# Kernel tuning notes

Hardware: AMD Instinct MI355X
Metric: run time of the kernel (lower is better)

## Reference

```python
import jax, jax.numpy as jnp
import numpy as np

N_NODES = 50000
N_EDGES = 640000
D = 128      # node feature dim
ED = 128     # edge feature dim
H = 128      # MLP hidden dim


def _glorot(key, shape):
    fan_in = shape[0]
    return jax.random.normal(key, shape, jnp.float32) * (1.0 / np.sqrt(fan_in))


def setup_inputs() -> dict:
    key = jax.random.key(0)
    ks = jax.random.split(key, 12)
    x = jax.random.normal(ks[0], (N_NODES, D), jnp.float32)
    edge_index = jax.random.randint(ks[1], (2, N_EDGES), 0, N_NODES, jnp.int64)
    edge_attr = jax.random.normal(ks[2], (N_EDGES, ED), jnp.float32)
    # edge_model: MLP on concat([src, dest, edge_attr]) -> ED
    We1 = _glorot(ks[3], (2 * D + ED, H)); be1 = jnp.zeros((H,), jnp.float32)
    We2 = _glorot(ks[4], (H, ED));         be2 = jnp.zeros((ED,), jnp.float32)
    # node_model: MLP on concat([x, scatter_mean(edge_attr, row)]) -> D
    Wn1 = _glorot(ks[5], (D + ED, H));     bn1 = jnp.zeros((H,), jnp.float32)
    Wn2 = _glorot(ks[6], (H, D));          bn2 = jnp.zeros((D,), jnp.float32)
    return {"x": x, "edge_index": edge_index, "edge_attr": edge_attr,
            "We1": We1, "be1": be1, "We2": We2, "be2": be2,
            "Wn1": Wn1, "bn1": bn1, "Wn2": Wn2, "bn2": bn2}


def reference(x, edge_index, edge_attr, We1, be1, We2, be2, Wn1, bn1, Wn2, bn2):
    row = edge_index[0]  # source / aggregation target, [E]
    col = edge_index[1]  # destination, [E]
    # edge_model(x[row], x[col], edge_attr): concat -> 2-layer ReLU MLP
    e_in = jnp.concatenate([x[row], x[col], edge_attr], axis=1)  # [E, 2D+ED]
    edge_out = jax.nn.relu(e_in @ We1 + be1) @ We2 + be2          # [E, ED]
    # node_model: scatter-mean of edge messages onto row nodes
    agg = jax.ops.segment_sum(edge_out, row, num_segments=N_NODES)         # [N, ED]
    cnt = jax.ops.segment_sum(jnp.ones((edge_out.shape[0], 1), x.dtype),
                              row, num_segments=N_NODES)                    # [N, 1]
    mean = agg / jnp.maximum(cnt, 1.0)
    n_in = jnp.concatenate([x, mean], axis=1)                     # [N, D+ED]
    x_out = jax.nn.relu(n_in @ Wn1 + bn1) @ Wn2 + bn2             # [N, D]
    return (x_out, edge_out)
```

## Files before the change

### kernel.cpp

```cpp
#include <hip/hip_runtime.h>
#include <stdint.h>


#define E_EDGES 640000
#define N_NODES 50000
#define DIM 128

typedef unsigned short u16;
typedef unsigned int u32x4 __attribute__((ext_vector_type(4)));
typedef float f32x4 __attribute__((ext_vector_type(4)));
typedef short s16x8 __attribute__((ext_vector_type(8)));
union U16 { u32x4 u; s16x8 s; u16 h[8]; };

__device__ __forceinline__ float b2f(u16 u) {
  union { unsigned i; float f; } v; v.i = ((unsigned)u) << 16; return v.f;
}
__device__ __forceinline__ u16 f2b(float f) {
  union { float f; unsigned u; } v; v.f = f;
  unsigned r = v.u + 0x7FFFu + ((v.u >> 16) & 1u);
  return (u16)(r >> 16);
}
__device__ __forceinline__ float ldf(const void* p, long long i, int isF32) {
  return isF32 ? ((const float*)p)[i] : b2f(((const u16*)p)[i]);
}

__global__ void detect_kernel(const void* x, const void* ei, int* flags) {
  __shared__ int sBig, sNz;
  if (threadIdx.x == 0) { sBig = 0; sNz = 0; }
  __syncthreads();
  const u16* xu = (const u16*)x;
  const int* ew = (const int*)ei;
  int big = 0, nz = 0;
  for (int i = threadIdx.x; i < 4096; i += 256) {
    u16 u = xu[2 * i];
    if (((u >> 7) & 0xFF) >= 0x90) big = 1;
    if (ew[2 * i + 1] != 0) nz = 1;
  }
  if (big) atomicOr(&sBig, 1);
  if (nz) atomicOr(&sNz, 1);
  __syncthreads();
  if (threadIdx.x == 0) { flags[0] = sBig; flags[1] = sNz ? 0 : 1; }
}

__global__ void normalize_idx(const void* ei, const int* __restrict__ flags,
                              int* __restrict__ out) {
  int i = blockIdx.x * 256 + threadIdx.x;
  if (flags[1]) out[i] = (int)((const long long*)ei)[i];
  else          out[i] = ((const int*)ei)[i];
}

__global__ void prep_weights(const void* We1, const void* be1, const void* We2,
                             const void* be2, const void* Wn1, const void* bn1,
                             const void* Wn2, const void* bn2,
                             const int* __restrict__ flags,
                             u16* __restrict__ WT1, u16* __restrict__ WT2,
                             u16* __restrict__ WnT1, u16* __restrict__ WnT2,
                             float* __restrict__ biasf) {
  const int isF32 = flags[0];
  int tid = blockIdx.x * 256 + threadIdx.x;
  if (tid < 384 * 128) { int k = tid >> 7, n = tid & 127; WT1 [n * 384 + k] = f2b(ldf(We1, tid, isF32)); }
  if (tid < 128 * 128) { int k = tid >> 7, n = tid & 127; WT2 [n * 128 + k] = f2b(ldf(We2, tid, isF32)); }
  if (tid < 256 * 128) { int k = tid >> 7, n = tid & 127; WnT1[n * 256 + k] = f2b(ldf(Wn1, tid, isF32)); }
  if (tid < 128 * 128) { int k = tid >> 7, n = tid & 127; WnT2[n * 128 + k] = f2b(ldf(Wn2, tid, isF32)); }
  if (tid < 128) {
    biasf[tid]       = ldf(be1, tid, isF32);
    biasf[128 + tid] = ldf(be2, tid, isF32);
    biasf[256 + tid] = ldf(bn1, tid, isF32);
    biasf[384 + tid] = ldf(bn2, tid, isF32);
  }
}

__global__ void convert_x(const void* x, const int* __restrict__ flags,
                          u16* __restrict__ xb) {
  int i = blockIdx.x * 256 + threadIdx.x;
  xb[i] = flags[0] ? f2b(((const float*)x)[i]) : ((const u16*)x)[i];
}

__global__ __launch_bounds__(256) void edge_kernel(
    const u16* __restrict__ xb, const int* __restrict__ ei, const void* ea,
    const u16* __restrict__ WT1, const u16* __restrict__ WT2,
    const float* __restrict__ biasf, const int* __restrict__ flags,
    void* d_out, float* __restrict__ agg, float* __restrict__ cnt) {
  __shared__ u16 h[4][32 * 136];
  const int isF32 = flags[0];
  const int wid = threadIdx.x >> 6, lane = threadIdx.x & 63;
  const int lm = lane & 15, quad = lane >> 4;
  const int ebase = (blockIdx.x * 4 + wid) * 32;

  if (threadIdx.x < 128)
    atomicAdd(&cnt[ei[blockIdx.x * 128 + threadIdx.x]], 1.0f);

  const int e0 = ebase + lm, e1 = ebase + 16 + lm;
  const int row0 = ei[e0], col0 = ei[E_EDGES + e0];
  const int row1 = ei[e1], col1 = ei[E_EDGES + e1];

  const f32x4 fz = {0.f, 0.f, 0.f, 0.f};
  f32x4 acc[2][8];
#pragma unroll
  for (int mt = 0; mt < 2; ++mt)
#pragma unroll
    for (int t = 0; t < 8; ++t) acc[mt][t] = fz;

#pragma unroll
  for (int ks = 0; ks < 12; ++ks) {
    const int k0 = ks * 32 + quad * 8;
    U16 a0, a1;
    if (k0 < 256) {
      const u16 *p0, *p1;
      if (k0 < 128) { p0 = xb + (size_t)row0 * DIM + k0;         p1 = xb + (size_t)row1 * DIM + k0; }
      else          { p0 = xb + (size_t)col0 * DIM + (k0 - 128); p1 = xb + (size_t)col1 * DIM + (k0 - 128); }
      a0.u = *(const u32x4*)p0;
      a1.u = *(const u32x4*)p1;
    } else {
      const int off = k0 - 256;
      if (isF32) {
        const float* q0 = (const float*)ea + (size_t)e0 * DIM + off;
        const float* q1 = (const float*)ea + (size_t)e1 * DIM + off;
        f32x4 lo0 = *(const f32x4*)q0, hi0 = *(const f32x4*)(q0 + 4);
        f32x4 lo1 = *(const f32x4*)q1, hi1 = *(const f32x4*)(q1 + 4);
#pragma unroll
        for (int j = 0; j < 4; ++j) {
          a0.h[j] = f2b(lo0[j]); a0.h[4 + j] = f2b(hi0[j]);
          a1.h[j] = f2b(lo1[j]); a1.h[4 + j] = f2b(hi1[j]);
        }
      } else {
        const u16* q0 = (const u16*)ea + (size_t)e0 * DIM + off;
        const u16* q1 = (const u16*)ea + (size_t)e1 * DIM + off;
        a0.u = *(const u32x4*)q0;
        a1.u = *(const u32x4*)q1;
      }
    }
#pragma unroll
    for (int t = 0; t < 8; ++t) {
      U16 b; b.u = *(const u32x4*)(WT1 + (t * 16 + lm) * 384 + k0);
      acc[0][t] = __builtin_amdgcn_mfma_f32_16x16x32_bf16(a0.s, b.s, acc[0][t], 0, 0, 0);
      acc[1][t] = __builtin_amdgcn_mfma_f32_16x16x32_bf16(a1.s, b.s, acc[1][t], 0, 0, 0);
    }
  }

  u16* hw = h[wid];
#pragma unroll
  for (int t = 0; t < 8; ++t) {
    const int n = t * 16 + lm;
    const float bias = biasf[n];
#pragma unroll
    for (int mt = 0; mt < 2; ++mt)
#pragma unroll
      for (int r = 0; r < 4; ++r) {
        float v = acc[mt][t][r] + bias;
        v = v > 0.f ? v : 0.f;
        hw[(mt * 16 + quad * 4 + r) * 136 + n] = f2b(v);
      }
  }
  __syncthreads();

  f32x4 acc2[2][8];
#pragma unroll
  for (int mt = 0; mt < 2; ++mt)
#pragma unroll
    for (int t = 0; t < 8; ++t) acc2[mt][t] = fz;

#pragma unroll
  for (int ks = 0; ks < 4; ++ks) {
    const int k0 = ks * 32 + quad * 8;
    U16 a0, a1;
    a0.u = *(const u32x4*)(hw + lm * 136 + k0);
    a1.u = *(const u32x4*)(hw + (16 + lm) * 136 + k0);
#pragma unroll
    for (int t = 0; t < 8; ++t) {
      U16 b; b.u = *(const u32x4*)(WT2 + (t * 16 + lm) * 128 + k0);
      acc2[0][t] = __builtin_amdgcn_mfma_f32_16x16x32_bf16(a0.s, b.s, acc2[0][t], 0, 0, 0);
      acc2[1][t] = __builtin_amdgcn_mfma_f32_16x16x32_bf16(a1.s, b.s, acc2[1][t], 0, 0, 0);
    }
  }

  int rowd[2][4];
#pragma unroll
  for (int mt = 0; mt < 2; ++mt)
#pragma unroll
    for (int r = 0; r < 4; ++r)
      rowd[mt][r] = ei[ebase + mt * 16 + quad * 4 + r];

  float* eoutf = (float*)d_out + (size_t)N_NODES * DIM;
  u16*   eoutb = (u16*)d_out   + (size_t)N_NODES * DIM;

#pragma unroll
  for (int t = 0; t < 8; ++t) {
    const int n = t * 16 + lm;
    const float bias = biasf[128 + n];
#pragma unroll
    for (int mt = 0; mt < 2; ++mt)
#pragma unroll
      for (int r = 0; r < 4; ++r) {
        float v = acc2[mt][t][r] + bias;
        const size_t e = (size_t)(ebase + mt * 16 + quad * 4 + r);
        atomicAdd(&agg[(size_t)rowd[mt][r] * DIM + n], v);
        if (isF32) eoutf[e * DIM + n] = v;
        else       eoutb[e * DIM + n] = f2b(v);
      }
  }
}

__global__ void mean_kernel(const float* __restrict__ agg,
                            const float* __restrict__ cnt,
                            u16* __restrict__ meanb) {
  int tid = blockIdx.x * 256 + threadIdx.x;
  float c = cnt[tid >> 7];
  meanb[tid] = f2b(agg[tid] / fmaxf(c, 1.0f));
}

__global__ __launch_bounds__(256) void node_kernel(
    const u16* __restrict__ xb, const u16* __restrict__ meanb,
    const u16* __restrict__ WnT1, const u16* __restrict__ WnT2,
    const float* __restrict__ biasf, const int* __restrict__ flags,
    void* d_out) {
  __shared__ u16 h[4][32 * 136];
  const int isF32 = flags[0];
  const int wid = threadIdx.x >> 6, lane = threadIdx.x & 63;
  const int lm = lane & 15, quad = lane >> 4;
  const int nbase = (blockIdx.x * 4 + wid) * 32;

  int nd0 = nbase + lm;      if (nd0 > N_NODES - 1) nd0 = N_NODES - 1;
  int nd1 = nbase + 16 + lm; if (nd1 > N_NODES - 1) nd1 = N_NODES - 1;

  const f32x4 fz = {0.f, 0.f, 0.f, 0.f};
  f32x4 acc[2][8];
#pragma unroll
  for (int mt = 0; mt < 2; ++mt)
#pragma unroll
    for (int t = 0; t < 8; ++t) acc[mt][t] = fz;

#pragma unroll
  for (int ks = 0; ks < 8; ++ks) {
    const int k0 = ks * 32 + quad * 8;
    const u16 *p0, *p1;
    if (k0 < 128) { p0 = xb + (size_t)nd0 * DIM + k0;            p1 = xb + (size_t)nd1 * DIM + k0; }
    else          { p0 = meanb + (size_t)nd0 * DIM + (k0 - 128); p1 = meanb + (size_t)nd1 * DIM + (k0 - 128); }
    U16 a0, a1;
    a0.u = *(const u32x4*)p0;
    a1.u = *(const u32x4*)p1;
#pragma unroll
    for (int t = 0; t < 8; ++t) {
      U16 b; b.u = *(const u32x4*)(WnT1 + (t * 16 + lm) * 256 + k0);
      acc[0][t] = __builtin_amdgcn_mfma_f32_16x16x32_bf16(a0.s, b.s, acc[0][t], 0, 0, 0);
      acc[1][t] = __builtin_amdgcn_mfma_f32_16x16x32_bf16(a1.s, b.s, acc[1][t], 0, 0, 0);
    }
  }

  u16* hw = h[wid];
#pragma unroll
  for (int t = 0; t < 8; ++t) {
    const int n = t * 16 + lm;
    const float bias = biasf[256 + n];
#pragma unroll
    for (int mt = 0; mt < 2; ++mt)
#pragma unroll
      for (int r = 0; r < 4; ++r) {
        float v = acc[mt][t][r] + bias;
        v = v > 0.f ? v : 0.f;
        hw[(mt * 16 + quad * 4 + r) * 136 + n] = f2b(v);
      }
  }
  __syncthreads();

  f32x4 acc2[2][8];
#pragma unroll
  for (int mt = 0; mt < 2; ++mt)
#pragma unroll
    for (int t = 0; t < 8; ++t) acc2[mt][t] = fz;

#pragma unroll
  for (int ks = 0; ks < 4; ++ks) {
    const int k0 = ks * 32 + quad * 8;
    U16 a0, a1;
    a0.u = *(const u32x4*)(hw + lm * 136 + k0);
    a1.u = *(const u32x4*)(hw + (16 + lm) * 136 + k0);
#pragma unroll
    for (int t = 0; t < 8; ++t) {
      U16 b; b.u = *(const u32x4*)(WnT2 + (t * 16 + lm) * 128 + k0);
      acc2[0][t] = __builtin_amdgcn_mfma_f32_16x16x32_bf16(a0.s, b.s, acc2[0][t], 0, 0, 0);
      acc2[1][t] = __builtin_amdgcn_mfma_f32_16x16x32_bf16(a1.s, b.s, acc2[1][t], 0, 0, 0);
    }
  }

  float* xoutf = (float*)d_out;
  u16*   xoutb = (u16*)d_out;
#pragma unroll
  for (int t = 0; t < 8; ++t) {
    const int n = t * 16 + lm;
    const float bias = biasf[384 + n];
#pragma unroll
    for (int mt = 0; mt < 2; ++mt)
#pragma unroll
      for (int r = 0; r < 4; ++r) {
        const int node = nbase + mt * 16 + quad * 4 + r;
        if (node < N_NODES) {
          float v = acc2[mt][t][r] + bias;
          if (isF32) xoutf[(size_t)node * DIM + n] = v;
          else       xoutb[(size_t)node * DIM + n] = f2b(v);
        }
      }
  }
}

extern "C" void kernel_launch(void* const* d_in, const int* in_sizes, int n_in,
                              void* d_out, int out_size, void* d_ws, size_t ws_size,
                              hipStream_t stream) {
  const void* x   = d_in[0];
  const void* ei  = d_in[1];
  const void* ea  = d_in[2];
  const void* We1 = d_in[3]; const void* be1 = d_in[4];
  const void* We2 = d_in[5]; const void* be2 = d_in[6];
  const void* Wn1 = d_in[7]; const void* bn1 = d_in[8];
  const void* Wn2 = d_in[9]; const void* bn2 = d_in[10];

  char* ws = (char*)d_ws;
  int*   flags  = (int*)(ws + 0);
  float* biasf  = (float*)(ws + 256);
  u16*   WT1    = (u16*)(ws + 4096);
  u16*   WT2    = (u16*)(ws + 102400);
  u16*   WnT1   = (u16*)(ws + 135168);
  u16*   WnT2   = (u16*)(ws + 200704);
  int*   eidx32 = (int*)(ws + 233472);
  float* agg    = (float*)(ws + 5353472);
  float* cnt    = (float*)(ws + 30953472);
  u16*   meanb  = (u16*)(ws + 31153472);
  u16*   xb     = (u16*)(ws + 43953472);

  hipMemsetAsync(ws + 5353472, 0, 25800000, stream);

  detect_kernel<<<1, 256, 0, stream>>>(x, ei, flags);
  normalize_idx<<<2 * E_EDGES / 256, 256, 0, stream>>>(ei, flags, eidx32);
  prep_weights<<<192, 256, 0, stream>>>(We1, be1, We2, be2, Wn1, bn1, Wn2, bn2,
                                        flags, WT1, WT2, WnT1, WnT2, biasf);
  convert_x<<<N_NODES * DIM / 256, 256, 0, stream>>>(x, flags, xb);
  edge_kernel<<<E_EDGES / 128, 256, 0, stream>>>(xb, eidx32, ea, WT1, WT2,
                                                 biasf, flags, d_out, agg, cnt);
  mean_kernel<<<N_NODES * DIM / 256, 256, 0, stream>>>(agg, cnt, meanb);
  node_kernel<<<(N_NODES + 127) / 128, 256, 0, stream>>>(xb, meanb, WnT1, WnT2,
                                                         biasf, flags, d_out);
}
```

Before: 1.115 ms.

## Replace atomic scatter-mean with CSR sort and per-node gather reduction

Instead of float atomics into a 50000x128 aggregation buffer from the edge kernel, the code builds a CSR grouping of edges by source row (histogram, single-block scan, scatter into a permutation). A new per-node kernel then gathers that node's edge outputs from the output buffer and writes the mean directly. This removes about 82M global float atomics and the large memset, but adds three preprocessing kernels, a serial single-block scan, and a re-read of the edge output. In the bf16 path the aggregation now sums rounded bf16 values, which slightly changes numerics.

```diff
diff --git a/kernel.cpp b/kernel.cpp
--- a/kernel.cpp
+++ b/kernel.cpp
@@ -9,6 +9,7 @@
 typedef unsigned short u16;
 typedef unsigned int u32x4 __attribute__((ext_vector_type(4)));
 typedef float f32x4 __attribute__((ext_vector_type(4)));
+typedef float f32x2 __attribute__((ext_vector_type(2)));
 typedef short s16x8 __attribute__((ext_vector_type(8)));
 union U16 { u32x4 u; s16x8 s; u16 h[8]; };
 
@@ -76,19 +77,60 @@
   xb[i] = flags[0] ? f2b(((const float*)x)[i]) : ((const u16*)x)[i];
 }
 
+__global__ void hist_kernel(const int* __restrict__ ei,
+                            int* __restrict__ ecnt) {
+  const int e = blockIdx.x * 256 + threadIdx.x;
+  atomicAdd(&ecnt[ei[e]], 1);
+}
+
+#define SCAN_CHUNK 196
+__global__ __launch_bounds__(256) void scan_kernel(
+    const int* __restrict__ ecnt, int* __restrict__ rowstart) {
+  __shared__ int sums[256];
+  __shared__ int pref[257];
+  const int t = threadIdx.x;
+  const int base = t * SCAN_CHUNK;
+  int s = 0;
+  for (int i = 0; i < SCAN_CHUNK; ++i) {
+    const int idx = base + i;
+    if (idx < N_NODES) s += ecnt[idx];
+  }
+  sums[t] = s;
+  __syncthreads();
+  if (t == 0) {
+    int run = 0;
+    for (int i = 0; i < 256; ++i) { pref[i] = run; run += sums[i]; }
+    pref[256] = run;
+  }
+  __syncthreads();
+  int run = pref[t];
+  for (int i = 0; i < SCAN_CHUNK; ++i) {
+    const int idx = base + i;
+    if (idx < N_NODES) { rowstart[idx] = run; run += ecnt[idx]; }
+  }
+  if (t == 0) rowstart[N_NODES] = pref[256];
+}
+
+__global__ void scatter_kernel(const int* __restrict__ ei,
+                               const int* __restrict__ rowstart,
+                               int* __restrict__ cursor,
+                               int* __restrict__ perm) {
+  const int e = blockIdx.x * 256 + threadIdx.x;
+  const int r = ei[e];
+  const int pos = rowstart[r] + atomicAdd(&cursor[r], 1);
+  perm[pos] = e;
+}
+
 __global__ __launch_bounds__(256) void edge_kernel(
     const u16* __restrict__ xb, const int* __restrict__ ei, const void* ea,
     const u16* __restrict__ WT1, const u16* __restrict__ WT2,
     const float* __restrict__ biasf, const int* __restrict__ flags,
-    void* d_out, float* __restrict__ agg, float* __restrict__ cnt) {
+    void* d_out) {
   __shared__ u16 h[4][32 * 136];
   const int isF32 = flags[0];
   const int wid = threadIdx.x >> 6, lane = threadIdx.x & 63;
   const int lm = lane & 15, quad = lane >> 4;
   const int ebase = (blockIdx.x * 4 + wid) * 32;
-
-  if (threadIdx.x < 128)
-    atomicAdd(&cnt[ei[blockIdx.x * 128 + threadIdx.x]], 1.0f);
 
   const int e0 = ebase + lm, e1 = ebase + 16 + lm;
   const int row0 = ei[e0], col0 = ei[E_EDGES + e0];
@@ -174,13 +216,6 @@
     }
   }
 
-  int rowd[2][4];
-#pragma unroll
-  for (int mt = 0; mt < 2; ++mt)
-#pragma unroll
-    for (int r = 0; r < 4; ++r)
-      rowd[mt][r] = ei[ebase + mt * 16 + quad * 4 + r];
-
   float* eoutf = (float*)d_out + (size_t)N_NODES * DIM;
   u16*   eoutb = (u16*)d_out   + (size_t)N_NODES * DIM;
 
@@ -194,19 +229,56 @@
       for (int r = 0; r < 4; ++r) {
         float v = acc2[mt][t][r] + bias;
         const size_t e = (size_t)(ebase + mt * 16 + quad * 4 + r);
-        atomicAdd(&agg[(size_t)rowd[mt][r] * DIM + n], v);
         if (isF32) eoutf[e * DIM + n] = v;
         else       eoutb[e * DIM + n] = f2b(v);
       }
   }
 }
 
-__global__ void mean_kernel(const float* __restrict__ agg,
-                            const float* __restrict__ cnt,
-                            u16* __restrict__ meanb) {
-  int tid = blockIdx.x * 256 + threadIdx.x;
-  float c = cnt[tid >> 7];
-  meanb[tid] = f2b(agg[tid] / fmaxf(c, 1.0f));
+__global__ __launch_bounds__(256) void agg_kernel(
+    const void* d_out, const int* __restrict__ rowstart,
+    const int* __restrict__ perm, const int* __restrict__ flags,
+    u16* __restrict__ meanb) {
+  const int isF32 = flags[0];
+  const int wid = threadIdx.x >> 6, lane = threadIdx.x & 63;
+  const int node = blockIdx.x * 4 + wid;
+  if (node >= N_NODES) return;
+  const int beg = rowstart[node], end = rowstart[node + 1];
+  float s0 = 0.f, s1 = 0.f;
+  if (isF32) {
+    const float* base = (const float*)d_out + (size_t)N_NODES * DIM;
+    int j = beg;
+    for (; j + 2 <= end; j += 2) {
+      const int ea0 = perm[j], ea1 = perm[j + 1];
+      const f32x2 v0 = *(const f32x2*)(base + (size_t)ea0 * DIM + lane * 2);
+      const f32x2 v1 = *(const f32x2*)(base + (size_t)ea1 * DIM + lane * 2);
+      s0 += v0.x + v1.x; s1 += v0.y + v1.y;
+    }
+    if (j < end) {
+      const int ea0 = perm[j];
+      const f32x2 v0 = *(const f32x2*)(base + (size_t)ea0 * DIM + lane * 2);
+      s0 += v0.x; s1 += v0.y;
+    }
+  } else {
+    const u16* base = (const u16*)d_out + (size_t)N_NODES * DIM;
+    int j = beg;
+    for (; j + 2 <= end; j += 2) {
+      const int ea0 = perm[j], ea1 = perm[j + 1];
+      const unsigned v0 = *(const unsigned*)(base + (size_t)ea0 * DIM + lane * 2);
+      const unsigned v1 = *(const unsigned*)(base + (size_t)ea1 * DIM + lane * 2);
+      s0 += b2f((u16)(v0 & 0xFFFF)) + b2f((u16)(v1 & 0xFFFF));
+      s1 += b2f((u16)(v0 >> 16)) + b2f((u16)(v1 >> 16));
+    }
+    if (j < end) {
+      const int ea0 = perm[j];
+      const unsigned v0 = *(const unsigned*)(base + (size_t)ea0 * DIM + lane * 2);
+      s0 += b2f((u16)(v0 & 0xFFFF));
+      s1 += b2f((u16)(v0 >> 16));
+    }
+  }
+  const float inv = 1.0f / fmaxf((float)(end - beg), 1.0f);
+  const unsigned out = ((unsigned)f2b(s1 * inv) << 16) | (unsigned)f2b(s0 * inv);
+  *(unsigned*)(meanb + (size_t)node * DIM + lane * 2) = out;
 }
 
 __global__ __launch_bounds__(256) void node_kernel(
@@ -315,28 +387,35 @@
   const void* Wn2 = d_in[9]; const void* bn2 = d_in[10];
 
   char* ws = (char*)d_ws;
-  int*   flags  = (int*)(ws + 0);
-  float* biasf  = (float*)(ws + 256);
-  u16*   WT1    = (u16*)(ws + 4096);
-  u16*   WT2    = (u16*)(ws + 102400);
-  u16*   WnT1   = (u16*)(ws + 135168);
-  u16*   WnT2   = (u16*)(ws + 200704);
-  int*   eidx32 = (int*)(ws + 233472);
-  float* agg    = (float*)(ws + 5353472);
-  float* cnt    = (float*)(ws + 30953472);
-  u16*   meanb  = (u16*)(ws + 31153472);
-  u16*   xb     = (u16*)(ws + 43953472);
-
-  hipMemsetAsync(ws + 5353472, 0, 25800000, stream);
+  int*   flags    = (int*)(ws + 0);
+  float* biasf    = (float*)(ws + 256);
+  u16*   WT1      = (u16*)(ws + 4096);
+  u16*   WT2      = (u16*)(ws + 102400);
+  u16*   WnT1     = (u16*)(ws + 135168);
+  u16*   WnT2     = (u16*)(ws + 200704);
+  int*   eidx32   = (int*)(ws + 233472);
+  int*   ecnt     = (int*)(ws + 5353472);
+  int*   cursor   = (int*)(ws + 5553472);
+  int*   rowstart = (int*)(ws + 5753472);
+  int*   perm     = (int*)(ws + 5953536);
+  u16*   meanb    = (u16*)(ws + 8513536);
+  u16*   xb       = (u16*)(ws + 21313536);
+
+  hipMemsetAsync(ws + 5353472, 0, 400000, stream);
 
   detect_kernel<<<1, 256, 0, stream>>>(x, ei, flags);
   normalize_idx<<<2 * E_EDGES / 256, 256, 0, stream>>>(ei, flags, eidx32);
   prep_weights<<<192, 256, 0, stream>>>(We1, be1, We2, be2, Wn1, bn1, Wn2, bn2,
                                         flags, WT1, WT2, WnT1, WnT2, biasf);
   convert_x<<<N_NODES * DIM / 256, 256, 0, stream>>>(x, flags, xb);
+
+  hist_kernel<<<E_EDGES / 256, 256, 0, stream>>>(eidx32, ecnt);
+  scan_kernel<<<1, 256, 0, stream>>>(ecnt, rowstart);
+  scatter_kernel<<<E_EDGES / 256, 256, 0, stream>>>(eidx32, rowstart, cursor, perm);
+
   edge_kernel<<<E_EDGES / 128, 256, 0, stream>>>(xb, eidx32, ea, WT1, WT2,
-                                                 biasf, flags, d_out, agg, cnt);
-  mean_kernel<<<N_NODES * DIM / 256, 256, 0, stream>>>(agg, cnt, meanb);
+                                                 biasf, flags, d_out);
+  agg_kernel<<<N_NODES / 4, 256, 0, stream>>>(d_out, rowstart, perm, flags, meanb);
   node_kernel<<<(N_NODES + 127) / 128, 256, 0, stream>>>(xb, meanb, WnT1, WnT2,
                                                          biasf, flags, d_out);
 }
```

Measured after the change: 1.177 ms. 5.5% more time.
